# Kernel optimization log

Measured on AMD Instinct MI355X. Metric: run time of the kernel, lower is better.

Reference implementation:

```python
import jax, jax.numpy as jnp
import numpy as np

# ---- static configuration (matches init_kwargs) ----
B, C, H, W = 32, 16, 128, 128
T_MIN, T_MAX, RES = 0.0, 1.0, 64
GH, GW = 2 * H - 1, 2 * W - 1              # vertex-mode cubical grid (gudhi all_cells)
SCALE = (RES - 1) / (T_MAX - T_MIN)

# Cell (i,j) in the (GH,GW) grid has corner vertices (i//2..(i+1)//2, j//2..(j+1)//2).
_i = np.arange(GH); _j = np.arange(GW)
I0, I1 = _i // 2, (_i + 1) // 2
J0, J1 = _j // 2, (_j + 1) // 2
_DIM = (_i % 2)[:, None] + (_j % 2)[None, :]          # 0=vertex, 1=edge, 2=square
SIGN = jnp.asarray(np.where(_DIM % 2 == 0, 1.0, -1.0), jnp.float32)  # (-1)**dim


def _cells(x):
    """x: [B,C,H,W] vertex values -> (corners [4,B,C,GH,GW], F [B,C,GH,GW]).
    Lower-star filtration: a cell's value is the max over its vertices."""
    c00 = x[..., I0[:, None], J0[None, :]]
    c01 = x[..., I0[:, None], J1[None, :]]
    c10 = x[..., I1[:, None], J0[None, :]]
    c11 = x[..., I1[:, None], J1[None, :]]
    corners = jnp.stack([c00, c01, c10, c11])
    return corners, corners.max(axis=0)


def setup_inputs() -> dict:
    key = jax.random.key(0)
    x = jax.random.uniform(key, (B, C, H, W), dtype=jnp.float32)
    return {"x": x}


def reference(x):
    """Euler characteristic curve of the sublevel cubical complex. Returns [B,C,RES]."""
    _, F = _cells(x)                                  # cell filtrations
    # bin index t = max(ceil((filt - t_min)*scale), 0); cells with filt > t_max skipped
    t = jnp.clip(jnp.ceil((F - T_MIN) * SCALE).astype(jnp.int32), 0, RES - 1)
    vals = SIGN * (F <= T_MAX).astype(jnp.float32)    # (-1)**dim masked
    bc, N = B * C, GH * GW
    idx = jnp.arange(bc, dtype=jnp.int32)[:, None] * RES + t.reshape(bc, N)
    hist = jnp.zeros(bc * RES, jnp.float32).at[idx.reshape(-1)].add(
        jnp.broadcast_to(vals, (B, C, GH, GW)).reshape(-1))
    return jnp.cumsum(hist.reshape(B, C, RES), axis=-1)
```

## Files before the change

kernel.cpp:

```cpp
#include <hip/hip_runtime.h>


#define BB 32
#define CC 16
#define HH 128
#define WW 128
#define RESB 64
#define NT 256
#define S 4
#define ROWS (HH / S)
#define RPT 4
#define BC (BB * CC)

__device__ __forceinline__ int binq(float F) {
    return (int)ceilf(F * 63.0f);
}

__global__ __launch_bounds__(NT, 5) void ecc_hist(const float* __restrict__ X,
                                                  int* __restrict__ ws) {
    __shared__ int hist[RESB * 32];
    const int blk = blockIdx.x;
    const int sl = blk & (S - 1);
    const int bc = blk >> 2;
    const int tid = threadIdx.x;
    const int ln = tid & 31;
    const float* __restrict__ x = X + (size_t)bc * (HH * WW);

    {
        int4* h4 = (int4*)hist;
        h4[tid] = make_int4(0, 0, 0, 0);
        h4[tid + NT] = make_int4(0, 0, 0, 0);
    }
    __syncthreads();

    const int col4 = tid & 31;
    const int tr = tid >> 5;
    const int r0 = sl * ROWS + tr * RPT;
    const int c0 = col4 * 4;
    const int cR = (col4 < 31) ? c0 + 4 : WW - 1;
    const int r4c = (r0 + 4 < HH) ? r0 + 4 : HH - 1;

    const float4 R0 = *(const float4*)(x + (r0 + 0) * WW + c0);
    const float4 R1 = *(const float4*)(x + (r0 + 1) * WW + c0);
    const float4 R2 = *(const float4*)(x + (r0 + 2) * WW + c0);
    const float4 R3 = *(const float4*)(x + (r0 + 3) * WW + c0);
    const float4 R4v = *(const float4*)(x + r4c * WW + c0);
    const float H0 = x[(r0 + 0) * WW + cR];
    const float H1 = x[(r0 + 1) * WW + cR];
    const float H2 = x[(r0 + 2) * WW + cR];
    const float H3 = x[(r0 + 3) * WW + cR];
    const float H4 = x[r4c * WW + cR];

    int bn[5][5];
    bn[0][0] = binq(R0.x); bn[0][1] = binq(R0.y); bn[0][2] = binq(R0.z); bn[0][3] = binq(R0.w); bn[0][4] = binq(H0);
    bn[1][0] = binq(R1.x); bn[1][1] = binq(R1.y); bn[1][2] = binq(R1.z); bn[1][3] = binq(R1.w); bn[1][4] = binq(H1);
    bn[2][0] = binq(R2.x); bn[2][1] = binq(R2.y); bn[2][2] = binq(R2.z); bn[2][3] = binq(R2.w); bn[2][4] = binq(H2);
    bn[3][0] = binq(R3.x); bn[3][1] = binq(R3.y); bn[3][2] = binq(R3.z); bn[3][3] = binq(R3.w); bn[3][4] = binq(H3);
    bn[4][0] = binq(R4v.x); bn[4][1] = binq(R4v.y); bn[4][2] = binq(R4v.z); bn[4][3] = binq(R4v.w); bn[4][4] = binq(H4);

    const int hD3 = (r0 + 3 < HH - 1) ? 1 : 0;

#pragma unroll
    for (int dr = 0; dr < RPT; ++dr) {
        const int hD = (dr < 3) ? 1 : hD3;
#pragma unroll
        for (int k = 0; k < 4; ++k) {
            const int hR = (k < 3) ? 1 : ((col4 < 31) ? 1 : 0);
            const int u00 = bn[dr][k];
            const int bh  = max(u00, bn[dr][k + 1]);
            const int bvv = max(u00, bn[dr + 1][k]);
            const int bf  = max(bh, max(bn[dr + 1][k], bn[dr + 1][k + 1]));
            atomicAdd(&hist[(u00 << 5) + ln], 1);
            atomicAdd(&hist[(bh  << 5) + ln], -hR);
            atomicAdd(&hist[(bvv << 5) + ln], -hD);
            atomicAdd(&hist[(bf  << 5) + ln], hR & hD);
        }
    }
    __syncthreads();

    const int bin = tid & 63;
    const int q = tid >> 6;
    int ssum = 0;
#pragma unroll
    for (int k = 0; k < 8; ++k) {
        ssum += hist[(bin << 5) + ((q * 8 + bin + k) & 31)];
    }
    __syncthreads();
    hist[tid] = ssum;
    __syncthreads();
    if (tid < RESB) {
        ws[blk * RESB + tid] = hist[tid] + hist[tid + 64] + hist[tid + 128] + hist[tid + 192];
    }
}

__global__ __launch_bounds__(64) void ecc_scan(const int* __restrict__ ws,
                                               float* __restrict__ out) {
    const int bc = blockIdx.x;
    const int b = threadIdx.x;
    int v = 0;
#pragma unroll
    for (int si = 0; si < S; ++si) v += ws[(bc * S + si) * RESB + b];
#pragma unroll
    for (int d = 1; d < 64; d <<= 1) {
        const int up = __shfl_up(v, d, 64);
        if (b >= d) v += up;
    }
    out[bc * RESB + b] = (float)v;
}

extern "C" void kernel_launch(void* const* d_in, const int* in_sizes, int n_in,
                              void* d_out, int out_size, void* d_ws, size_t ws_size,
                              hipStream_t stream) {
    const float* x = (const float*)d_in[0];
    float* out = (float*)d_out;
    int* ws = (int*)d_ws;
    ecc_hist<<<BC * S, NT, 0, stream>>>(x, ws);
    ecc_scan<<<BC, 64, 0, stream>>>(ws, out);
}
```

Baseline: 13.81 us.

## Attribute each cell to its argmax vertex, one LDS atomic per pixel

Instead of binning each vertex, edge and square separately with four shared-memory atomics per pixel, each cell is assigned to the unique vertex that attains its max, using index-based tie-breaking via strict and non-strict comparisons. Each pixel then computes a signed weight from its 3x3 neighbourhood and does a single atomic add at its own bin. This cuts LDS atomics fourfold at the cost of loading a 6x6 halo (more global loads), doing extra comparisons, and relying on the tie-breaking rules being consistent.

Result: slower. 16.69 us (+20.9%).

```diff
diff --git a/kernel.cpp b/kernel.cpp
--- a/kernel.cpp
+++ b/kernel.cpp
@@ -37,43 +37,45 @@
     const int tr = tid >> 5;
     const int r0 = sl * ROWS + tr * RPT;
     const int c0 = col4 * 4;
-    const int cR = (col4 < 31) ? c0 + 4 : WW - 1;
-    const int r4c = (r0 + 4 < HH) ? r0 + 4 : HH - 1;
+    const int cL = (c0 > 0) ? c0 - 1 : 0;
+    const int cR = (c0 + 4 < WW) ? c0 + 4 : WW - 1;
 
-    const float4 R0 = *(const float4*)(x + (r0 + 0) * WW + c0);
-    const float4 R1 = *(const float4*)(x + (r0 + 1) * WW + c0);
-    const float4 R2 = *(const float4*)(x + (r0 + 2) * WW + c0);
-    const float4 R3 = *(const float4*)(x + (r0 + 3) * WW + c0);
-    const float4 R4v = *(const float4*)(x + r4c * WW + c0);
-    const float H0 = x[(r0 + 0) * WW + cR];
-    const float H1 = x[(r0 + 1) * WW + cR];
-    const float H2 = x[(r0 + 2) * WW + cR];
-    const float H3 = x[(r0 + 3) * WW + cR];
-    const float H4 = x[r4c * WW + cR];
+    float Fr[6][6];
+#pragma unroll
+    for (int j = 0; j < 6; ++j) {
+        int rr = r0 - 1 + j;
+        rr = rr < 0 ? 0 : (rr > HH - 1 ? HH - 1 : rr);
+        const float* rp = x + rr * WW;
+        const float4 a = *(const float4*)(rp + c0);
+        Fr[j][1] = a.x; Fr[j][2] = a.y; Fr[j][3] = a.z; Fr[j][4] = a.w;
+        Fr[j][0] = rp[cL];
+        Fr[j][5] = rp[cR];
+    }
 
-    int bn[5][5];
-    bn[0][0] = binq(R0.x); bn[0][1] = binq(R0.y); bn[0][2] = binq(R0.z); bn[0][3] = binq(R0.w); bn[0][4] = binq(H0);
-    bn[1][0] = binq(R1.x); bn[1][1] = binq(R1.y); bn[1][2] = binq(R1.z); bn[1][3] = binq(R1.w); bn[1][4] = binq(H1);
-    bn[2][0] = binq(R2.x); bn[2][1] = binq(R2.y); bn[2][2] = binq(R2.z); bn[2][3] = binq(R2.w); bn[2][4] = binq(H2);
-    bn[3][0] = binq(R3.x); bn[3][1] = binq(R3.y); bn[3][2] = binq(R3.z); bn[3][3] = binq(R3.w); bn[3][4] = binq(H3);
-    bn[4][0] = binq(R4v.x); bn[4][1] = binq(R4v.y); bn[4][2] = binq(R4v.z); bn[4][3] = binq(R4v.w); bn[4][4] = binq(H4);
-
+    const int hl0 = (col4 > 0) ? 1 : 0;
+    const int hr3 = (col4 < 31) ? 1 : 0;
+    const int hU0 = (r0 > 0) ? 1 : 0;
     const int hD3 = (r0 + 3 < HH - 1) ? 1 : 0;
 
 #pragma unroll
     for (int dr = 0; dr < RPT; ++dr) {
+        const int hU = (dr > 0) ? 1 : hU0;
         const int hD = (dr < 3) ? 1 : hD3;
 #pragma unroll
         for (int k = 0; k < 4; ++k) {
-            const int hR = (k < 3) ? 1 : ((col4 < 31) ? 1 : 0);
-            const int u00 = bn[dr][k];
-            const int bh  = max(u00, bn[dr][k + 1]);
-            const int bvv = max(u00, bn[dr + 1][k]);
-            const int bf  = max(bh, max(bn[dr + 1][k], bn[dr + 1][k + 1]));
-            atomicAdd(&hist[(u00 << 5) + ln], 1);
-            atomicAdd(&hist[(bh  << 5) + ln], -hR);
-            atomicAdd(&hist[(bvv << 5) + ln], -hD);
-            atomicAdd(&hist[(bf  << 5) + ln], hR & hD);
+            const int hl = (k > 0) ? 1 : hl0;
+            const int hr = (k < 3) ? 1 : hr3;
+            const float xv = Fr[dr + 1][k + 1];
+            const int pL = hl & (Fr[dr + 1][k] <= xv ? 1 : 0);
+            const int pR = hr & (Fr[dr + 1][k + 2] < xv ? 1 : 0);
+            const int pU = hU & (Fr[dr][k + 1] <= xv ? 1 : 0);
+            const int pD = hD & (Fr[dr + 2][k + 1] < xv ? 1 : 0);
+            const int fUL = pU & pL & (Fr[dr][k] <= xv ? 1 : 0);
+            const int fUR = pU & pR & (Fr[dr][k + 2] <= xv ? 1 : 0);
+            const int fDL = pD & pL & (Fr[dr + 2][k] < xv ? 1 : 0);
+            const int fDR = pD & pR & (Fr[dr + 2][k + 2] < xv ? 1 : 0);
+            const int w = 1 - pL - pR - pU - pD + fUL + fUR + fDL + fDR;
+            atomicAdd(&hist[(binq(xv) << 5) + ln], w);
         }
     }
     __syncthreads();
```
